# Kernel optimization log

Hardware: AMD Instinct MI355X
Metric: run time of the kernel (lower is better)

## Reference

```python
import jax, jax.numpy as jnp
import numpy as np

SIZE = 2048
BATCH = 4096


def setup_inputs() -> dict:
    key = jax.random.key(0)
    ks = jax.random.split(key, 7)
    s = 1.0 / np.sqrt(SIZE)  # torch Linear default init scale
    return {
        "x": jax.random.normal(ks[0], (BATCH, SIZE), dtype=jnp.float32),
        "h": jax.random.normal(ks[1], (BATCH, SIZE), dtype=jnp.float32),
        "c": jax.random.normal(ks[2], (BATCH, SIZE), dtype=jnp.float32),
        # gate order: i, f, o, c_candidate; torch Linear weights are (out, in)
        "Wx": jax.random.uniform(ks[3], (4, SIZE, SIZE), jnp.float32, -s, s),
        "bx": jax.random.uniform(ks[4], (4, SIZE), jnp.float32, -s, s),
        "Wh": jax.random.uniform(ks[5], (4, SIZE, SIZE), jnp.float32, -s, s),
        "bh": jax.random.uniform(ks[6], (4, SIZE), jnp.float32, -s, s),
    }


def reference(x, h, c, Wx, bx, Wh, bh):
    # Fused form of the 8 separate Linears: two batched GEMMs (x-side, h-side)
    # gates: (4, B, S) in order i, f, o, c_
    gates = (jnp.einsum('bi,goi->gbo', x, Wx) + bx[:, None, :]
             + jnp.einsum('bi,goi->gbo', h, Wh) + bh[:, None, :])
    i = jax.nn.sigmoid(gates[0])
    f = jax.nn.sigmoid(gates[1])
    o = jax.nn.sigmoid(gates[2])
    c_ = jnp.tanh(gates[3])
    c_new = f * c + i * c_
    h_new = o * jnp.tanh(c_new)
    return (h_new, c_new)
```

## Files before the change

### kernel.cpp

```cpp
#include <hip/hip_runtime.h>


typedef __bf16 bf16;
typedef __attribute__((ext_vector_type(8))) __bf16 bf16x8;
typedef __attribute__((ext_vector_type(4))) float f32x4;

#define BATCH 4096
#define SIZE  2048
#define KCAT  4096
#define NTOT  8192
#define BM 128
#define BN 128
#define BK 32

__device__ __forceinline__ bf16 f2bf(float f) {
    unsigned u = __builtin_bit_cast(unsigned, f);
    u += 0x7fffu + ((u >> 16) & 1u);
    unsigned short h = (unsigned short)(u >> 16);
    return __builtin_bit_cast(bf16, h);
}

__device__ __forceinline__ void gld_lds16(const bf16* g, bf16* l) {
    __builtin_amdgcn_global_load_lds(
        (__attribute__((address_space(1))) void*)(const_cast<bf16*>(g)),
        (__attribute__((address_space(3))) void*)l,
        16, 0, 0);
}

template <int MODE>
__global__ __launch_bounds__(256) void cast_concat(
    const float* __restrict__ srcA, const float* __restrict__ srcB,
    bf16* __restrict__ dst)
{
    long t = (long)blockIdx.x * 256 + threadIdx.x;
    long e = t << 3;
    long nprime = e >> 12;
    int  col    = (int)(e & 4095);
    long srow;
    if (MODE == 0) {
        srow = nprime;
    } else {
        int t16 = (int)(nprime & 15);
        int g   = (int)((nprime >> 4) & 3);
        long s  = ((nprime >> 6) << 4) + t16;
        srow = (long)g * SIZE + s;
    }
    const float* src = (col < SIZE) ? (srcA + (srow << 11) + col)
                                    : (srcB + (srow << 11) + (col - SIZE));
    f32x4 v0 = *(const f32x4*)src;
    f32x4 v1 = *(const f32x4*)(src + 4);
    bf16x8 o;
    o[0] = f2bf(v0[0]); o[1] = f2bf(v0[1]); o[2] = f2bf(v0[2]); o[3] = f2bf(v0[3]);
    o[4] = f2bf(v1[0]); o[5] = f2bf(v1[1]); o[6] = f2bf(v1[2]); o[7] = f2bf(v1[3]);
    *(bf16x8*)(dst + e) = o;
}

__device__ __forceinline__ float sigm(float x) {
    return 1.f / (1.f + __expf(-x));
}
__device__ __forceinline__ float tanh_fast(float x) {
    float e = __expf(2.f * x);
    return 1.f - 2.f / (e + 1.f);
}

__global__ __launch_bounds__(256) void gemm_lstm(
    const bf16* __restrict__ A, const bf16* __restrict__ W,
    const float* __restrict__ bx, const float* __restrict__ bh,
    const float* __restrict__ c, float* __restrict__ out)
{
    __shared__ __align__(16) bf16 sA[BM * BK];
    __shared__ __align__(16) bf16 sB[BN * BK];

    const int tid  = threadIdx.x;
    const int lane = tid & 63;
    const int wave = tid >> 6;
    const int wm   = wave >> 1;
    const int wn   = wave & 1;

    const int m0 = blockIdx.y * BM;
    const int n0 = blockIdx.x * BN;

    const int selem = tid * 8;
    const int srow  = tid >> 2;
    const int scol  = (tid & 3) * 8;
    const bf16* gA0 = A + (size_t)(m0 + srow) * KCAT + scol;
    const bf16* gB0 = W + (size_t)(n0 + srow) * KCAT + scol;

    f32x4 acc[4][4];
#pragma unroll
    for (int i = 0; i < 4; i++)
#pragma unroll
        for (int j = 0; j < 4; j++)
            acc[i][j] = (f32x4){0.f, 0.f, 0.f, 0.f};

    const int fra = wm * 64 + (lane & 15);
    const int frb = wn * 64 + (lane & 15);
    const int frk = (lane >> 4) * 8;

    gld_lds16(gA0,                     &sA[selem]);
    gld_lds16(gA0 + (size_t)64 * KCAT, &sA[selem + 2048]);
    gld_lds16(gB0,                     &sB[selem]);
    gld_lds16(gB0 + (size_t)64 * KCAT, &sB[selem + 2048]);

    const int NK = KCAT / BK;
    for (int kt = 0; kt < NK; ++kt) {
        __syncthreads();

        bf16x8 a[4], b[4];
#pragma unroll
        for (int i = 0; i < 4; i++)
            a[i] = *(const bf16x8*)&sA[(fra + i * 16) * BK + frk];
#pragma unroll
        for (int j = 0; j < 4; j++)
            b[j] = *(const bf16x8*)&sB[(frb + j * 16) * BK + frk];

        __syncthreads();

        if (kt + 1 < NK) {
            const bf16* ga = gA0 + (size_t)(kt + 1) * BK;
            const bf16* gb = gB0 + (size_t)(kt + 1) * BK;
            gld_lds16(ga,                     &sA[selem]);
            gld_lds16(ga + (size_t)64 * KCAT, &sA[selem + 2048]);
            gld_lds16(gb,                     &sB[selem]);
            gld_lds16(gb + (size_t)64 * KCAT, &sB[selem + 2048]);
        }

#pragma unroll
        for (int i = 0; i < 4; i++)
#pragma unroll
            for (int j = 0; j < 4; j++)
                acc[i][j] = __builtin_amdgcn_mfma_f32_16x16x32_bf16(
                    a[i], b[j], acc[i][j], 0, 0, 0);
    }

    const int s = blockIdx.x * 32 + wn * 16 + (lane & 15);
    const float b_i = bx[0 * SIZE + s] + bh[0 * SIZE + s];
    const float b_f = bx[1 * SIZE + s] + bh[1 * SIZE + s];
    const float b_o = bx[2 * SIZE + s] + bh[2 * SIZE + s];
    const float b_c = bx[3 * SIZE + s] + bh[3 * SIZE + s];

    const int row0 = m0 + wm * 64 + (lane >> 4) * 4;
    float* hout = out;
    float* cout = out + (size_t)BATCH * SIZE;

#pragma unroll
    for (int i = 0; i < 4; i++) {
#pragma unroll
        for (int r = 0; r < 4; r++) {
            const int row = row0 + i * 16 + r;
            const size_t idx = (size_t)row * SIZE + s;
            float i_ = sigm(acc[i][0][r] + b_i);
            float f_ = sigm(acc[i][1][r] + b_f);
            float o_ = sigm(acc[i][2][r] + b_o);
            float cc = tanh_fast(acc[i][3][r] + b_c);
            float cn = f_ * c[idx] + i_ * cc;
            hout[idx] = o_ * tanh_fast(cn);
            cout[idx] = cn;
        }
    }
}

extern "C" void kernel_launch(void* const* d_in, const int* in_sizes, int n_in,
                              void* d_out, int out_size, void* d_ws, size_t ws_size,
                              hipStream_t stream) {
    const float* x  = (const float*)d_in[0];
    const float* h  = (const float*)d_in[1];
    const float* c  = (const float*)d_in[2];
    const float* Wx = (const float*)d_in[3];
    const float* bx = (const float*)d_in[4];
    const float* Wh = (const float*)d_in[5];
    const float* bh = (const float*)d_in[6];
    float* out = (float*)d_out;

    char* w = (char*)d_ws;
    bf16* Acat = (bf16*)w;
    bf16* Wcat = (bf16*)(w + (size_t)33554432);

    cast_concat<0><<<(BATCH * (size_t)KCAT / 8) / 256, 256, 0, stream>>>(
        x, h, Acat);
    cast_concat<1><<<(NTOT * (size_t)KCAT / 8) / 256, 256, 0, stream>>>(
        Wx, Wh, Wcat);

    dim3 grid(NTOT / BN, BATCH / BM);
    gemm_lstm<<<grid, 256, 0, stream>>>(Acat, Wcat, bx, bh, c, out);
}
```

Before: 580.0 us.

## Rewrite LSTM GEMM as 256x256 double-buffered tile with swizzled LDS and XCD remap

Replaces the 128x128x32 single-buffered GEMM with a 256x256x64 tile run by 8 waves. It uses double-buffered LDS (128KB), XOR-swizzled LDS columns to avoid bank conflicts, and interleaves global-to-LDS prefetch with four MFMA phases using barriers and s_setprio. Blocks are remapped so neighbouring tiles land on the same XCD for L2 reuse. The goal is to hide load latency and raise arithmetic intensity. The cost is heavy register pressure from 32 accumulators per lane and 128KB of LDS, which limits occupancy to one block per CU.

```diff
diff --git a/kernel.cpp b/kernel.cpp
--- a/kernel.cpp
+++ b/kernel.cpp
@@ -9,9 +9,10 @@
 #define SIZE  2048
 #define KCAT  4096
 #define NTOT  8192
-#define BM 128
-#define BN 128
-#define BK 32
+#define BM 256
+#define BN 256
+#define BK 64
+#define NT (KCAT / BK)
 
 __device__ __forceinline__ bf16 f2bf(float f) {
     unsigned u = __builtin_bit_cast(unsigned, f);
@@ -63,96 +64,169 @@
     return 1.f - 2.f / (e + 1.f);
 }
 
-__global__ __launch_bounds__(256) void gemm_lstm(
+#define MFMA16(ai, bj, cij) \
+    cij = __builtin_amdgcn_mfma_f32_16x16x32_bf16(ai, bj, cij, 0, 0, 0)
+
+__global__ __launch_bounds__(512, 2) void gemm_lstm(
     const bf16* __restrict__ A, const bf16* __restrict__ W,
-    const float* __restrict__ bx, const float* __restrict__ bh,
+    const float* __restrict__ bxg, const float* __restrict__ bhg,
     const float* __restrict__ c, float* __restrict__ out)
 {
-    __shared__ __align__(16) bf16 sA[BM * BK];
-    __shared__ __align__(16) bf16 sB[BN * BK];
+    __shared__ __align__(16) bf16 sAB[65536];
 
     const int tid  = threadIdx.x;
     const int lane = tid & 63;
     const int wave = tid >> 6;
-    const int wm   = wave >> 1;
-    const int wn   = wave & 1;
-
-    const int m0 = blockIdx.y * BM;
-    const int n0 = blockIdx.x * BN;
-
-    const int selem = tid * 8;
-    const int srow  = tid >> 2;
-    const int scol  = (tid & 3) * 8;
-    const bf16* gA0 = A + (size_t)(m0 + srow) * KCAT + scol;
-    const bf16* gB0 = W + (size_t)(n0 + srow) * KCAT + scol;
-
-    f32x4 acc[4][4];
-#pragma unroll
-    for (int i = 0; i < 4; i++)
+    const int wm   = wave >> 2;
+    const int wn   = wave & 3;
+
+    const int orig = blockIdx.x;
+    const int xcd  = orig & 7;
+    const int loc  = orig >> 3;
+    const int bxt  = (xcd & 3) * 8 + (loc & 7);
+    const int byt  = (xcd >> 2) * 8 + (loc >> 3);
+    const int m0 = byt * BM;
+    const int n0 = bxt * BN;
+
+    const int grow0 = tid >> 3;
+    const int colE  = (((tid & 7) ^ (grow0 & 7)) << 3);
+    const bf16* pA = A + (size_t)(m0 + grow0) * KCAT + colE;
+    const bf16* pB = W + (size_t)(n0 + grow0) * KCAT + colE;
+
+#define STAGE_A(t, h) do {                                                   \
+        const bf16* _g = pA + (size_t)(h) * (128 * KCAT) + (size_t)(t) * BK; \
+        const int _l = (((t) & 1) << 14) + ((h) << 13) + tid * 8;            \
+        gld_lds16(_g,                     &sAB[_l]);                         \
+        gld_lds16(_g + (size_t)64 * KCAT, &sAB[_l + 4096]);                  \
+    } while (0)
+#define STAGE_B(t, h) do {                                                   \
+        const bf16* _g = pB + (size_t)(h) * (128 * KCAT) + (size_t)(t) * BK; \
+        const int _l = 32768 + (((t) & 1) << 14) + ((h) << 13) + tid * 8;    \
+        gld_lds16(_g,                     &sAB[_l]);                         \
+        gld_lds16(_g + (size_t)64 * KCAT, &sAB[_l + 4096]);                  \
+    } while (0)
+
+    const int l15   = lane & 15;
+    const int swzX  = (lane & 7) << 4;
+    const int cSwz0 = (( (lane >> 4) << 4)        ^ swzX) >> 1;
+    const int cSwz1 = ((64 | ((lane >> 4) << 4))  ^ swzX) >> 1;
+    const int aR = l15 * 64;
+    const int bR = ((wn & 1) * 64 + l15) * 64;
+
+    f32x4 acc[8][4];
+#pragma unroll
+    for (int i = 0; i < 8; i++)
 #pragma unroll
         for (int j = 0; j < 4; j++)
             acc[i][j] = (f32x4){0.f, 0.f, 0.f, 0.f};
 
-    const int fra = wm * 64 + (lane & 15);
-    const int frb = wn * 64 + (lane & 15);
-    const int frk = (lane >> 4) * 8;
-
-    gld_lds16(gA0,                     &sA[selem]);
-    gld_lds16(gA0 + (size_t)64 * KCAT, &sA[selem + 2048]);
-    gld_lds16(gB0,                     &sB[selem]);
-    gld_lds16(gB0 + (size_t)64 * KCAT, &sB[selem + 2048]);
-
-    const int NK = KCAT / BK;
-    for (int kt = 0; kt < NK; ++kt) {
-        __syncthreads();
-
-        bf16x8 a[4], b[4];
-#pragma unroll
-        for (int i = 0; i < 4; i++)
-            a[i] = *(const bf16x8*)&sA[(fra + i * 16) * BK + frk];
-#pragma unroll
-        for (int j = 0; j < 4; j++)
-            b[j] = *(const bf16x8*)&sB[(frb + j * 16) * BK + frk];
-
-        __syncthreads();
-
-        if (kt + 1 < NK) {
-            const bf16* ga = gA0 + (size_t)(kt + 1) * BK;
-            const bf16* gb = gB0 + (size_t)(kt + 1) * BK;
-            gld_lds16(ga,                     &sA[selem]);
-            gld_lds16(ga + (size_t)64 * KCAT, &sA[selem + 2048]);
-            gld_lds16(gb,                     &sB[selem]);
-            gld_lds16(gb + (size_t)64 * KCAT, &sB[selem + 2048]);
-        }
-
-#pragma unroll
-        for (int i = 0; i < 4; i++)
-#pragma unroll
-            for (int j = 0; j < 4; j++)
-                acc[i][j] = __builtin_amdgcn_mfma_f32_16x16x32_bf16(
-                    a[i], b[j], acc[i][j], 0, 0, 0);
+    STAGE_A(0, 0); STAGE_A(0, 1); STAGE_B(0, 0); STAGE_B(0, 1);
+    STAGE_B(1, 0); STAGE_B(1, 1);
+    asm volatile("s_waitcnt vmcnt(4)" ::: "memory");
+    __builtin_amdgcn_s_barrier();
+
+    for (int t = 0; t < NT; ++t) {
+        const int aBase = ((t & 1) << 14) + (wm << 13);
+        const int bBase = 32768 + ((t & 1) << 14) + ((wn >> 1) << 13);
+        bf16x8 a[4][2], b[4][2];
+
+#pragma unroll
+        for (int i = 0; i < 4; ++i) {
+            a[i][0] = *(const bf16x8*)&sAB[aBase + i * 1024 + aR + cSwz0];
+            a[i][1] = *(const bf16x8*)&sAB[aBase + i * 1024 + aR + cSwz1];
+        }
+#pragma unroll
+        for (int j = 0; j < 2; ++j) {
+            b[j][0] = *(const bf16x8*)&sAB[bBase + j * 1024 + bR + cSwz0];
+            b[j][1] = *(const bf16x8*)&sAB[bBase + j * 1024 + bR + cSwz1];
+        }
+        if (t + 1 < NT) STAGE_A(t + 1, 0);
+        __builtin_amdgcn_s_barrier();
+        __builtin_amdgcn_s_setprio(1);
+#pragma unroll
+        for (int i = 0; i < 4; ++i)
+#pragma unroll
+            for (int j = 0; j < 2; ++j) {
+                MFMA16(a[i][0], b[j][0], acc[i][j]);
+                MFMA16(a[i][1], b[j][1], acc[i][j]);
+            }
+        __builtin_amdgcn_s_setprio(0);
+        __builtin_amdgcn_s_barrier();
+
+#pragma unroll
+        for (int j = 2; j < 4; ++j) {
+            b[j][0] = *(const bf16x8*)&sAB[bBase + j * 1024 + bR + cSwz0];
+            b[j][1] = *(const bf16x8*)&sAB[bBase + j * 1024 + bR + cSwz1];
+        }
+        if (t + 1 < NT) STAGE_A(t + 1, 1);
+        __builtin_amdgcn_s_barrier();
+        __builtin_amdgcn_s_setprio(1);
+#pragma unroll
+        for (int i = 0; i < 4; ++i)
+#pragma unroll
+            for (int j = 2; j < 4; ++j) {
+                MFMA16(a[i][0], b[j][0], acc[i][j]);
+                MFMA16(a[i][1], b[j][1], acc[i][j]);
+            }
+        __builtin_amdgcn_s_setprio(0);
+        __builtin_amdgcn_s_barrier();
+
+#pragma unroll
+        for (int i = 0; i < 4; ++i) {
+            a[i][0] = *(const bf16x8*)&sAB[aBase + (4 + i) * 1024 + aR + cSwz0];
+            a[i][1] = *(const bf16x8*)&sAB[aBase + (4 + i) * 1024 + aR + cSwz1];
+        }
+        if (t + 2 < NT) STAGE_B(t + 2, 0);
+        __builtin_amdgcn_s_barrier();
+        __builtin_amdgcn_s_setprio(1);
+#pragma unroll
+        for (int i = 0; i < 4; ++i)
+#pragma unroll
+            for (int j = 2; j < 4; ++j) {
+                MFMA16(a[i][0], b[j][0], acc[4 + i][j]);
+                MFMA16(a[i][1], b[j][1], acc[4 + i][j]);
+            }
+        __builtin_amdgcn_s_setprio(0);
+        __builtin_amdgcn_s_barrier();
+
+        if (t + 2 < NT) STAGE_B(t + 2, 1);
+        __builtin_amdgcn_s_barrier();
+        __builtin_amdgcn_s_setprio(1);
+#pragma unroll
+        for (int i = 0; i < 4; ++i)
+#pragma unroll
+            for (int j = 0; j < 2; ++j) {
+                MFMA16(a[i][0], b[j][0], acc[4 + i][j]);
+                MFMA16(a[i][1], b[j][1], acc[4 + i][j]);
+            }
+        __builtin_amdgcn_s_setprio(0);
+        if (t + 2 < NT) asm volatile("s_waitcnt vmcnt(4)" ::: "memory");
+        else            asm volatile("s_waitcnt vmcnt(0)" ::: "memory");
+        __builtin_amdgcn_s_barrier();
     }
-
-    const int s = blockIdx.x * 32 + wn * 16 + (lane & 15);
-    const float b_i = bx[0 * SIZE + s] + bh[0 * SIZE + s];
-    const float b_f = bx[1 * SIZE + s] + bh[1 * SIZE + s];
-    const float b_o = bx[2 * SIZE + s] + bh[2 * SIZE + s];
-    const float b_c = bx[3 * SIZE + s] + bh[3 * SIZE + s];
-
-    const int row0 = m0 + wm * 64 + (lane >> 4) * 4;
+#undef STAGE_A
+#undef STAGE_B
+
+    const int s   = (bxt * 4 + wn) * 16 + l15;
+    const float b_i = bxg[0 * SIZE + s] + bhg[0 * SIZE + s];
+    const float b_f = bxg[1 * SIZE + s] + bhg[1 * SIZE + s];
+    const float b_o = bxg[2 * SIZE + s] + bhg[2 * SIZE + s];
+    const float b_c = bxg[3 * SIZE + s] + bhg[3 * SIZE + s];
+
+    const int row0 = m0 + wm * 128 + (lane >> 4) * 4;
     float* hout = out;
     float* cout = out + (size_t)BATCH * SIZE;
 
 #pragma unroll
-    for (int i = 0; i < 4; i++) {
-#pragma unroll
-        for (int r = 0; r < 4; r++) {
-            const int row = row0 + i * 16 + r;
+    for (int mi = 0; mi < 8; ++mi) {
+#pragma unroll
+        for (int r = 0; r < 4; ++r) {
+            const int row = row0 + mi * 16 + r;
             const size_t idx = (size_t)row * SIZE + s;
-            float i_ = sigm(acc[i][0][r] + b_i);
-            float f_ = sigm(acc[i][1][r] + b_f);
-            float o_ = sigm(acc[i][2][r] + b_o);
-            float cc = tanh_fast(acc[i][3][r] + b_c);
+            float i_ = sigm(acc[mi][0][r] + b_i);
+            float f_ = sigm(acc[mi][1][r] + b_f);
+            float o_ = sigm(acc[mi][2][r] + b_o);
+            float cc = tanh_fast(acc[mi][3][r] + b_c);
             float cn = f_ * c[idx] + i_ * cc;
             hout[idx] = o_ * tanh_fast(cn);
             cout[idx] = cn;
@@ -181,6 +255,5 @@
     cast_concat<1><<<(NTOT * (size_t)KCAT / 8) / 256, 256, 0, stream>>>(
         Wx, Wh, Wcat);
 
-    dim3 grid(NTOT / BN, BATCH / BM);
-    gemm_lstm<<<grid, 256, 0, stream>>>(Acat, Wcat, bx, bh, c, out);
-}
+    gemm_lstm<<<dim3(512), 512, 0, stream>>>(Acat, Wcat, bx, bh, c, out);
+}
```

After: 465.8 us. 19.7% less time.
